# Performance work log

Measured on AMD Instinct MI355X. Metric: run time of the kernel, lower is better.

## Reference

```python
import jax, jax.numpy as jnp
import numpy as np

EMB = 1024
HEADS = 16
HEADSIZE = EMB // HEADS


def _layernorm(x, gamma, beta, eps=1e-5):
    # LayerNorm over the last dim (headsize), affine.
    mu = jnp.mean(x, axis=-1, keepdims=True)
    var = jnp.var(x, axis=-1, keepdims=True)
    return (x - mu) * jax.lax.rsqrt(var + eps) * gamma + beta


def setup_inputs() -> dict:
    key = jax.random.key(0)
    ks = jax.random.split(key, 12)
    B, TI, TC = 4, 1024, 1024
    s = 1.0 / np.sqrt(EMB)
    inp = {
        "x": jax.random.normal(ks[0], (B, TI, EMB), dtype=jnp.float32),
        "context": jax.random.normal(ks[1], (B, TC, EMB), dtype=jnp.float32),
        # torch nn.Linear weights are (out, in); y = x @ W.T
        "Wq": jax.random.uniform(ks[2], (EMB, EMB), jnp.float32, -s, s),
        "Wk": jax.random.uniform(ks[3], (EMB, EMB), jnp.float32, -s, s),
        "Wv": jax.random.uniform(ks[4], (EMB, EMB), jnp.float32, -s, s),
        "Wu": jax.random.uniform(ks[5], (EMB, EMB), jnp.float32, -s, s),
        "bu": jax.random.uniform(ks[6], (EMB,), jnp.float32, -s, s),
        "q_gamma": jnp.ones((HEADSIZE,), jnp.float32),
        "q_beta": jnp.zeros((HEADSIZE,), jnp.float32),
        "k_gamma": jnp.ones((HEADSIZE,), jnp.float32),
        "k_beta": jnp.zeros((HEADSIZE,), jnp.float32),
    }
    return inp


def reference(x, context, Wq, Wk, Wv, Wu, bu, q_gamma, q_beta, k_gamma, k_beta):
    B, TI, E = x.shape
    TC = context.shape[1]
    T = TI + TC
    xc = jnp.concatenate([x, context], axis=1)  # [B, T, E]

    q = (x @ Wq.T).reshape(B, TI, HEADS, HEADSIZE)
    k = (xc @ Wk.T).reshape(B, T, HEADS, HEADSIZE)
    v = (xc @ Wv.T).reshape(B, T, HEADS, HEADSIZE)

    # optional QK-LayerNorm over headsize
    q = _layernorm(q, q_gamma, q_beta)
    k = _layernorm(k, k_gamma, k_beta)

    scale = E ** 0.25
    q = q / scale
    k = k / scale

    # scores: [B, H, TI, T]
    dot = jnp.einsum("bihd,bjhd->bhij", q, k)
    attn = jax.nn.softmax(dot, axis=-1)
    out = jnp.einsum("bhij,bjhd->bihd", attn, v).reshape(B, TI, E)
    return out @ Wu.T + bu
```

## Files before the change

### kernel.cpp

```cpp
#include <hip/hip_runtime.h>
#include <cstdint>


typedef unsigned short u16;
typedef __attribute__((ext_vector_type(8))) short bf16x8;
typedef __attribute__((ext_vector_type(4))) float f32x4;
typedef __attribute__((ext_vector_type(16))) float f32x16;
typedef __attribute__((ext_vector_type(4))) unsigned short u16x4;
typedef __attribute__((ext_vector_type(2))) unsigned int u32x2;

#define GLDS(gsrc, ldst)                                                              \
  __builtin_amdgcn_global_load_lds(                                                   \
      (const __attribute__((address_space(1))) unsigned int*)(gsrc),                  \
      (__attribute__((address_space(3))) unsigned int*)(ldst), 16, 0, 0)

__device__ __forceinline__ u16 f2bf(float x) {
  unsigned int u = __float_as_uint(x);
  u += 0x7fffu + ((u >> 16) & 1u);
  return (u16)(u >> 16);
}

__device__ __forceinline__ unsigned cvt_pk_bf16(float lo, float hi) {
  unsigned r;
  asm("v_cvt_pk_bf16_f32 %0, %1, %2" : "=v"(r) : "v"(lo), "v"(hi));
  return r;
}

__device__ __forceinline__ f32x4 mfma16(bf16x8 a, bf16x8 b, f32x4 c) {
  return __builtin_amdgcn_mfma_f32_16x16x32_bf16(a, b, c, 0, 0, 0);
}
__device__ __forceinline__ f32x16 mfma32(bf16x8 a, bf16x8 b, f32x16 c) {
  return __builtin_amdgcn_mfma_f32_32x32x16_bf16(a, b, c, 0, 0, 0);
}


__global__ __launch_bounds__(256) void cast_concat(const float* __restrict__ x,
                                                   const float* __restrict__ c,
                                                   u16* __restrict__ o) {
  const int n4 = (8 << 20) / 4;
  for (int i = blockIdx.x * blockDim.x + threadIdx.x; i < n4; i += gridDim.x * blockDim.x) {
    int elem = i * 4;
    int b = elem >> 21;
    int rem = elem & ((1 << 21) - 1);
    int r = rem >> 10;
    int e = rem & 1023;
    const float* src = (r < 1024) ? (x + ((((size_t)(b << 10)) + r) << 10) + e)
                                  : (c + ((((size_t)(b << 10)) + (r - 1024)) << 10) + e);
    float4 v = *(const float4*)src;
    u16x4 ov;
    ov.x = f2bf(v.x); ov.y = f2bf(v.y); ov.z = f2bf(v.z); ov.w = f2bf(v.w);
    *(u16x4*)(o + elem) = ov;
  }
}

__global__ __launch_bounds__(256) void cast_w(const float* __restrict__ w0,
                                              const float* __restrict__ w1,
                                              const float* __restrict__ w2,
                                              const float* __restrict__ w3,
                                              u16* __restrict__ o) {
  const int n4 = (4 << 20) / 4;
  for (int i = blockIdx.x * blockDim.x + threadIdx.x; i < n4; i += gridDim.x * blockDim.x) {
    int elem = i * 4;
    int sel = elem >> 20;
    int loc = elem & ((1 << 20) - 1);
    const float* s = (sel == 0) ? w0 : (sel == 1) ? w1 : (sel == 2) ? w2 : w3;
    float4 v = *(const float4*)(s + loc);
    u16x4 ov;
    ov.x = f2bf(v.x); ov.y = f2bf(v.y); ov.z = f2bf(v.z); ov.w = f2bf(v.w);
    *(u16x4*)(o + elem) = ov;
  }
}


__global__ __launch_bounds__(256)
void gemm_qkv(const u16* __restrict__ XCB, const u16* __restrict__ Wall,
              u16* __restrict__ QBB, u16* __restrict__ KBB, u16* __restrict__ VT,
              const float* __restrict__ qg, const float* __restrict__ qb,
              const float* __restrict__ kg, const float* __restrict__ kb,
              float sQ, float sK) {
  const int ny = blockIdx.y;
  const int which = ny >> 3;
  const int m0 = blockIdx.x << 7;
  if (which == 0 && (m0 & 2047) >= 1024) return;
  const int n0 = (ny & 7) << 7;
  const u16* Bw = Wall + ((size_t)which << 20);
  const int K = 1024, N = 1024;

  __shared__ alignas(16) u16 lA[2][128 * 32];
  __shared__ alignas(16) u16 lB[2][128 * 32];
  const int tid = threadIdx.x;
  const int wv = tid >> 6, l = tid & 63, g = l >> 4, c16 = l & 15;
  const int wr = wv >> 1, wc = wv & 1;

  f32x4 acc[4][4];
  const f32x4 z4 = {0.f, 0.f, 0.f, 0.f};
#pragma unroll
  for (int i = 0; i < 4; ++i)
#pragma unroll
    for (int j = 0; j < 4; ++j) acc[i][j] = z4;

  const int srow = tid >> 2;
  const int scA = (tid & 3) ^ (srow & 3);
  const u16* aSrc = XCB + (size_t)(m0 + srow) * K + scA * 8;
  const u16* bSrc = Bw + (size_t)(n0 + srow) * K + scA * 8;
  char* ldA = (char*)lA;
  char* ldB = (char*)lB;
  const int lof = wv * 1024;

#define STAGE_G(bi, kof)                                   \
  {                                                        \
    char* dA = ldA + (bi)*8192 + lof;                      \
    char* dB = ldB + (bi)*8192 + lof;                      \
    GLDS(aSrc + (kof), dA);                                \
    GLDS(aSrc + (size_t)64 * K + (kof), dA + 4096);        \
    GLDS(bSrc + (kof), dB);                                \
    GLDS(bSrc + (size_t)64 * K + (kof), dB + 4096);        \
  }

  STAGE_G(0, 0);
  __syncthreads();
  int buf = 0;
  for (int kt = 0; kt < 32; ++kt) {
    if (kt + 1 < 32) STAGE_G(buf ^ 1, (kt + 1) << 5);
    const char* bA = ldA + buf * 8192;
    const char* bB = ldB + buf * 8192;
    bf16x8 af[4], bfr[4];
#pragma unroll
    for (int mi = 0; mi < 4; ++mi) {
      int row = wr * 64 + mi * 16 + c16;
      af[mi] = *(const bf16x8*)(bA + row * 64 + ((g * 16) ^ ((row & 3) << 4)));
    }
#pragma unroll
    for (int ni = 0; ni < 4; ++ni) {
      int row = wc * 64 + ni * 16 + c16;
      bfr[ni] = *(const bf16x8*)(bB + row * 64 + ((g * 16) ^ ((row & 3) << 4)));
    }
    __builtin_amdgcn_s_setprio(1);
#pragma unroll
    for (int mi = 0; mi < 4; ++mi)
#pragma unroll
      for (int ni = 0; ni < 4; ++ni)
        acc[mi][ni] = mfma16(af[mi], bfr[ni], acc[mi][ni]);
    __builtin_amdgcn_s_setprio(0);
    __syncthreads();
    buf ^= 1;
  }
#undef STAGE_G

  if (which == 2) {
#pragma unroll
    for (int ni = 0; ni < 4; ++ni) {
      int col = n0 + wc * 64 + ni * 16 + c16;
      int hh = col >> 6, dd = col & 63;
#pragma unroll
      for (int mi = 0; mi < 4; ++mi) {
        int m = m0 + wr * 64 + mi * 16 + g * 4;
        int bb = m >> 11, tt = m & 2047;
        u16x4 o;
#pragma unroll
        for (int r = 0; r < 4; ++r) o[r] = f2bf(acc[mi][ni][r]);
        *(u16x4*)(VT + ((size_t)((bb * 16 + hh) * 64 + dd)) * 2048 + tt) = o;
      }
    }
  } else {
    const float* G = which ? kg : qg;
    const float* Bt = which ? kb : qb;
    const float osc = which ? sK : sQ;
    u16* Ob = which ? KBB : QBB;
#pragma unroll
    for (int mi = 0; mi < 4; ++mi) {
      float sum[4], sq[4];
#pragma unroll
      for (int r = 0; r < 4; ++r) {
        float s = 0.f, q = 0.f;
#pragma unroll
        for (int ni = 0; ni < 4; ++ni) {
          float v = acc[mi][ni][r];
          s += v;
          q += v * v;
        }
#pragma unroll
        for (int msk = 1; msk < 16; msk <<= 1) {
          s += __shfl_xor(s, msk);
          q += __shfl_xor(q, msk);
        }
        sum[r] = s;
        sq[r] = q;
      }
#pragma unroll
      for (int ni = 0; ni < 4; ++ni) {
        int dloc = ni * 16 + c16;
        int colg = n0 + wc * 64 + ni * 16 + c16;
        float gv = G[dloc], bv = Bt[dloc];
#pragma unroll
        for (int r = 0; r < 4; ++r) {
          float mean = sum[r] * (1.f / 64.f);
          float var = sq[r] * (1.f / 64.f) - mean * mean;
          float y = (acc[mi][ni][r] - mean) * rsqrtf(var + 1e-5f) * gv + bv;
          int row = m0 + wr * 64 + mi * 16 + g * 4 + r;
          int orow = which ? row : (((row >> 11) << 10) | (row & 1023));
          Ob[(size_t)orow * N + colg] = f2bf(y * osc);
        }
      }
    }
  }
}


__global__ __launch_bounds__(256)
void gemm_u64(const u16* __restrict__ A, const u16* __restrict__ Bw,
              float* __restrict__ Of, const float* __restrict__ bias) {
  const int K = 1024, N = 1024;
  __shared__ alignas(16) u16 lA[2][64 * 32];
  __shared__ alignas(16) u16 lB[2][128 * 32];
  const int tid = threadIdx.x;
  const int wv = tid >> 6, l = tid & 63, g = l >> 4, c16 = l & 15;
  const int wr = wv >> 1, wc = wv & 1;
  const int m0 = blockIdx.x << 6, n0 = blockIdx.y << 7;

  f32x4 acc[2][4];
  const f32x4 z4 = {0.f, 0.f, 0.f, 0.f};
#pragma unroll
  for (int i = 0; i < 2; ++i)
#pragma unroll
    for (int j = 0; j < 4; ++j) acc[i][j] = z4;

  const int srow = tid >> 2;
  const int sc = (tid & 3) ^ (srow & 3);
  const u16* aSrc = A + (size_t)(m0 + srow) * K + sc * 8;
  const u16* bSrc = Bw + (size_t)(n0 + srow) * K + sc * 8;
  char* ldA = (char*)lA;
  char* ldB = (char*)lB;
  const int lof = wv * 1024;

#define STAGE_U(bi, kof)                                   \
  {                                                        \
    char* dA = ldA + (bi)*4096 + lof;                      \
    char* dB = ldB + (bi)*8192 + lof;                      \
    GLDS(aSrc + (kof), dA);                                \
    GLDS(bSrc + (kof), dB);                                \
    GLDS(bSrc + (size_t)64 * K + (kof), dB + 4096);        \
  }

  STAGE_U(0, 0);
  __syncthreads();
  int buf = 0;
  for (int kt = 0; kt < 32; ++kt) {
    if (kt + 1 < 32) STAGE_U(buf ^ 1, (kt + 1) << 5);
    const char* bA = ldA + buf * 4096;
    const char* bB = ldB + buf * 8192;
    bf16x8 af[2], bfr[4];
#pragma unroll
    for (int mi = 0; mi < 2; ++mi) {
      int row = wr * 32 + mi * 16 + c16;
      af[mi] = *(const bf16x8*)(bA + row * 64 + ((g * 16) ^ ((row & 3) << 4)));
    }
#pragma unroll
    for (int ni = 0; ni < 4; ++ni) {
      int row = wc * 64 + ni * 16 + c16;
      bfr[ni] = *(const bf16x8*)(bB + row * 64 + ((g * 16) ^ ((row & 3) << 4)));
    }
    __builtin_amdgcn_s_setprio(1);
#pragma unroll
    for (int mi = 0; mi < 2; ++mi)
#pragma unroll
      for (int ni = 0; ni < 4; ++ni)
        acc[mi][ni] = mfma16(af[mi], bfr[ni], acc[mi][ni]);
    __builtin_amdgcn_s_setprio(0);
    __syncthreads();
    buf ^= 1;
  }
#undef STAGE_U

#pragma unroll
  for (int ni = 0; ni < 4; ++ni) {
    int col = n0 + wc * 64 + ni * 16 + c16;
    float bv = bias[col];
#pragma unroll
    for (int mi = 0; mi < 2; ++mi) {
      int row = m0 + wr * 32 + mi * 16 + g * 4;
      float* dst = Of + (size_t)row * N + col;
#pragma unroll
      for (int r = 0; r < 4; ++r) dst[(size_t)r * N] = acc[mi][ni][r] + bv;
    }
  }
}


__global__ __launch_bounds__(512, 4)
void attn_kernel(const u16* __restrict__ Q, const u16* __restrict__ Kb,
                 const u16* __restrict__ Vt, u16* __restrict__ AO) {
  __shared__ union alignas(16) {
    struct { u16 K[2][2][4096]; u16 V[2][2][4096]; } kv;
    float cmb[4][64][34];
  } sm;
  const int tid = threadIdx.x;
  const int wv = tid >> 6, l = tid & 63;
  const int w4 = wv & 3, kvh2 = wv >> 2;
  const int lq = l & 31, hi = l >> 5;
  const int b = blockIdx.z, h = blockIdx.y, qt = blockIdx.x;
  const int qrow = (b << 10) + (qt << 7) + (w4 << 5) + lq;

  const u16* qp = Q + (size_t)qrow * 1024 + h * 64 + hi * 8;
  bf16x8 qf[4];
#pragma unroll
  for (int kk = 0; kk < 4; ++kk) qf[kk] = *(const bf16x8*)(qp + 16 * kk);

  f32x16 acc[2];
#pragma unroll
  for (int d0 = 0; d0 < 2; ++d0)
#pragma unroll
    for (int i = 0; i < 16; ++i) acc[d0][i] = 0.f;
  float m_run = -1e30f, l_run = 0.f;

  const u16* Ksrc = Kb + ((size_t)(b * 2048) + l) * 1024 + h * 64 + w4 * 8;
  const u16* Vsrc = Vt + ((size_t)((b * 16 + h) * 64) + l) * 2048 + w4 * 8;

#define STAGE_KV(bi, it)                                    \
  {                                                         \
    const int kv0 = ((it) << 7) + (kvh2 << 6);              \
    char* dK = (char*)sm.kv.K[kvh2][bi] + w4 * 1024;        \
    char* dV = (char*)sm.kv.V[kvh2][bi] + w4 * 1024;        \
    const u16* ks = Ksrc + (size_t)kv0 * 1024;              \
    const u16* vs = Vsrc + kv0;                             \
    GLDS(ks, dK);                                           \
    GLDS(ks + 32, dK + 4096);                               \
    GLDS(vs, dV);                                           \
    GLDS(vs + 32, dV + 4096);                               \
  }

  STAGE_KV(0, 0);
  __syncthreads();
  int buf = 0;

  for (int it = 0; it < 16; ++it) {
    if (it + 1 < 16) STAGE_KV(buf ^ 1, it + 1);
    const char* bK = (const char*)sm.kv.K[kvh2][buf];
    const char* bV = (const char*)sm.kv.V[kvh2][buf];

    f32x16 s[2];
#pragma unroll
    for (int kvh = 0; kvh < 2; ++kvh)
#pragma unroll
      for (int i = 0; i < 16; ++i) s[kvh][i] = 0.f;
    __builtin_amdgcn_s_setprio(1);
#pragma unroll
    for (int kk = 0; kk < 4; ++kk) {
      const char* kbase = bK + (2 * kk + hi) * 1024;
      bf16x8 kf0 = *(const bf16x8*)(kbase + lq * 16);
      bf16x8 kf1 = *(const bf16x8*)(kbase + (32 + lq) * 16);
      s[0] = mfma32(kf0, qf[kk], s[0]);
      s[1] = mfma32(kf1, qf[kk], s[1]);
    }
    __builtin_amdgcn_s_setprio(0);

    float tm0 = fmaxf(s[0][0], s[1][0]), tm1 = fmaxf(s[0][1], s[1][1]);
    float tm2 = fmaxf(s[0][2], s[1][2]), tm3 = fmaxf(s[0][3], s[1][3]);
#pragma unroll
    for (int i = 4; i < 16; i += 4) {
      tm0 = fmaxf(tm0, fmaxf(s[0][i], s[1][i]));
      tm1 = fmaxf(tm1, fmaxf(s[0][i + 1], s[1][i + 1]));
      tm2 = fmaxf(tm2, fmaxf(s[0][i + 2], s[1][i + 2]));
      tm3 = fmaxf(tm3, fmaxf(s[0][i + 3], s[1][i + 3]));
    }
    float tm = fmaxf(fmaxf(tm0, tm1), fmaxf(tm2, tm3));
    tm = fmaxf(tm, __shfl_xor(tm, 32));
    if (!__all(tm <= m_run + 8.f)) {
      float mnew = fmaxf(m_run, tm);
      float corr = __builtin_amdgcn_exp2f(m_run - mnew);
      l_run *= corr;
#pragma unroll
      for (int d0 = 0; d0 < 2; ++d0)
#pragma unroll
        for (int i = 0; i < 16; ++i) acc[d0][i] *= corr;
      m_run = mnew;
    }
    float ts0 = 0.f, ts1 = 0.f, ts2 = 0.f, ts3 = 0.f;
#pragma unroll
    for (int kvh = 0; kvh < 2; ++kvh)
#pragma unroll
      for (int i = 0; i < 16; i += 4) {
        float p0 = __builtin_amdgcn_exp2f(s[kvh][i] - m_run);
        float p1 = __builtin_amdgcn_exp2f(s[kvh][i + 1] - m_run);
        float p2 = __builtin_amdgcn_exp2f(s[kvh][i + 2] - m_run);
        float p3 = __builtin_amdgcn_exp2f(s[kvh][i + 3] - m_run);
        s[kvh][i] = p0; s[kvh][i + 1] = p1; s[kvh][i + 2] = p2; s[kvh][i + 3] = p3;
        ts0 += p0; ts1 += p1; ts2 += p2; ts3 += p3;
      }
    float ts = (ts0 + ts1) + (ts2 + ts3);
    ts += __shfl_xor(ts, 32);
    l_run += ts;

    unsigned int pk[2][4][2];
#pragma unroll
    for (int kvh = 0; kvh < 2; ++kvh)
#pragma unroll
      for (int kp = 0; kp < 4; ++kp)
#pragma unroll
        for (int tt = 0; tt < 2; ++tt)
          pk[kvh][kp][tt] = cvt_pk_bf16(s[kvh][4 * kp + 2 * tt], s[kvh][4 * kp + 2 * tt + 1]);

    __builtin_amdgcn_s_setprio(1);
#pragma unroll
    for (int kk = 0; kk < 4; ++kk) {
      const int kvh = kk >> 1, kb = kk & 1;
      union { unsigned w[4]; bf16x8 v; } bw;
#pragma unroll
      for (int tt = 0; tt < 2; ++tt) {
        unsigned A0 = pk[kvh][2 * kb][tt];
        unsigned A1 = pk[kvh][2 * kb + 1][tt];
        unsigned S = (unsigned)__shfl_xor((int)(hi ? A0 : A1), 32);
        bw.w[tt] = hi ? S : A0;
        bw.w[2 + tt] = hi ? A1 : S;
      }
      const char* vbase = bV + (2 * kk + hi) * 1024;
      bf16x8 vf0 = *(const bf16x8*)(vbase + lq * 16);
      bf16x8 vf1 = *(const bf16x8*)(vbase + (32 + lq) * 16);
      acc[0] = mfma32(vf0, bw.v, acc[0]);
      acc[1] = mfma32(vf1, bw.v, acc[1]);
    }
    __builtin_amdgcn_s_setprio(0);
    __syncthreads();
    buf ^= 1;
  }
#undef STAGE_KV

  if (wv >= 4) {
    float* cp = sm.cmb[w4][l];
#pragma unroll
    for (int d0 = 0; d0 < 2; ++d0)
#pragma unroll
      for (int i = 0; i < 16; ++i) cp[d0 * 16 + i] = acc[d0][i];
    cp[32] = m_run;
    cp[33] = l_run;
  }
  __syncthreads();
  if (wv < 4) {
    const float* cp = sm.cmb[w4][l];
    float m1 = cp[32], l1 = cp[33];
    float mm = fmaxf(m_run, m1);
    float c0 = __builtin_amdgcn_exp2f(m_run - mm);
    float c1 = __builtin_amdgcn_exp2f(m1 - mm);
    float invl = 1.f / (l_run * c0 + l1 * c1);
    float s0 = c0 * invl, s1 = c1 * invl;
#pragma unroll
    for (int d0 = 0; d0 < 2; ++d0)
#pragma unroll
      for (int rg = 0; rg < 4; ++rg) {
        float v0 = acc[d0][4 * rg + 0] * s0 + cp[d0 * 16 + 4 * rg + 0] * s1;
        float v1 = acc[d0][4 * rg + 1] * s0 + cp[d0 * 16 + 4 * rg + 1] * s1;
        float v2 = acc[d0][4 * rg + 2] * s0 + cp[d0 * 16 + 4 * rg + 2] * s1;
        float v3 = acc[d0][4 * rg + 3] * s0 + cp[d0 * 16 + 4 * rg + 3] * s1;
        u32x2 o;
        o.x = cvt_pk_bf16(v0, v1);
        o.y = cvt_pk_bf16(v2, v3);
        int d = 32 * d0 + 8 * rg + 4 * hi;
        *(u32x2*)(AO + (size_t)qrow * 1024 + h * 64 + d) = o;
      }
  }
}


extern "C" void kernel_launch(void* const* d_in, const int* in_sizes, int n_in,
                              void* d_out, int out_size, void* d_ws, size_t ws_size,
                              hipStream_t stream) {
  const float* x = (const float*)d_in[0];
  const float* ctx = (const float*)d_in[1];
  const float* Wq = (const float*)d_in[2];
  const float* Wk = (const float*)d_in[3];
  const float* Wv = (const float*)d_in[4];
  const float* Wu = (const float*)d_in[5];
  const float* bu = (const float*)d_in[6];
  const float* qg = (const float*)d_in[7];
  const float* qb = (const float*)d_in[8];
  const float* kg = (const float*)d_in[9];
  const float* kb = (const float*)d_in[10];
  float* out = (float*)d_out;

  char* w = (char*)d_ws;
  u16* XCB = (u16*)(w);
  u16* WQB = (u16*)(w + ((size_t)16 << 20));
  u16* QBB = (u16*)(w + ((size_t)24 << 20));
  u16* KBB = (u16*)(w + ((size_t)32 << 20));
  u16* VT = (u16*)(w + ((size_t)48 << 20));
  u16* AO = (u16*)(w + ((size_t)64 << 20));

  const float invs = 0.17677669529663687f;
  const float invs_l2e = invs * 1.44269504088896f;

  cast_concat<<<2048, 256, 0, stream>>>(x, ctx, XCB);
  cast_w<<<1024, 256, 0, stream>>>(Wq, Wk, Wv, Wu, WQB);

  gemm_qkv<<<dim3(64, 24), 256, 0, stream>>>(XCB, WQB, QBB, KBB, VT,
                                             qg, qb, kg, kb, invs_l2e, invs);

  attn_kernel<<<dim3(8, 16, 4), 512, 0, stream>>>(QBB, KBB, VT, AO);

  gemm_u64<<<dim3(64, 8), 256, 0, stream>>>(AO, WQB + ((size_t)3 << 20), out, bu);
}
```

Baseline: 276.5 us.

## Triple-buffer GEMM LDS staging with vmcnt waits and k-major LDS layout; reorder attention grid

Both projection GEMMs now stage three K-tiles in LDS instead of two. They issue loads two steps ahead and wait with explicit s_waitcnt vmcnt plus a single barrier per iteration, rather than two __syncthreads. The LDS layout moves from swizzled row-major to k-chunk-major, where each wave writes one 8-element k-slice for 64 rows, so fragment reads no longer need the XOR swizzle. The attention grid is reordered so heads vary fastest, with the aim of improving K/V cache reuse across neighbouring blocks. The extra buffer uses more LDS, which may limit occupancy, and the new layout may bring back bank conflicts.

```diff
diff --git a/kernel.cpp b/kernel.cpp
--- a/kernel.cpp
+++ b/kernel.cpp
@@ -86,8 +86,8 @@
   const u16* Bw = Wall + ((size_t)which << 20);
   const int K = 1024, N = 1024;
 
-  __shared__ alignas(16) u16 lA[2][128 * 32];
-  __shared__ alignas(16) u16 lB[2][128 * 32];
+  __shared__ alignas(16) u16 lAm[3][128 * 32];
+  __shared__ alignas(16) u16 lBm[3][128 * 32];
   const int tid = threadIdx.x;
   const int wv = tid >> 6, l = tid & 63, g = l >> 4, c16 = l & 15;
   const int wr = wv >> 1, wc = wv & 1;
@@ -99,42 +99,41 @@
 #pragma unroll
     for (int j = 0; j < 4; ++j) acc[i][j] = z4;
 
-  const int srow = tid >> 2;
-  const int scA = (tid & 3) ^ (srow & 3);
-  const u16* aSrc = XCB + (size_t)(m0 + srow) * K + scA * 8;
-  const u16* bSrc = Bw + (size_t)(n0 + srow) * K + scA * 8;
-  char* ldA = (char*)lA;
-  char* ldB = (char*)lB;
-  const int lof = wv * 1024;
+  const u16* aSrc = XCB + (size_t)(m0 + l) * K + wv * 8;
+  const u16* bSrc = Bw + (size_t)(n0 + l) * K + wv * 8;
+  char* ldA = (char*)lAm;
+  char* ldB = (char*)lBm;
 
 #define STAGE_G(bi, kof)                                   \
   {                                                        \
-    char* dA = ldA + (bi)*8192 + lof;                      \
-    char* dB = ldB + (bi)*8192 + lof;                      \
+    char* dA = ldA + (bi)*8192 + wv * 2048;                \
+    char* dB = ldB + (bi)*8192 + wv * 2048;                \
     GLDS(aSrc + (kof), dA);                                \
-    GLDS(aSrc + (size_t)64 * K + (kof), dA + 4096);        \
+    GLDS(aSrc + (size_t)64 * K + (kof), dA + 1024);        \
     GLDS(bSrc + (kof), dB);                                \
-    GLDS(bSrc + (size_t)64 * K + (kof), dB + 4096);        \
+    GLDS(bSrc + (size_t)64 * K + (kof), dB + 1024);        \
   }
 
   STAGE_G(0, 0);
-  __syncthreads();
-  int buf = 0;
+  STAGE_G(1, 32);
+  int cb = 0, sb = 2;
   for (int kt = 0; kt < 32; ++kt) {
-    if (kt + 1 < 32) STAGE_G(buf ^ 1, (kt + 1) << 5);
-    const char* bA = ldA + buf * 8192;
-    const char* bB = ldB + buf * 8192;
+    if (kt < 31) {
+      asm volatile("s_waitcnt vmcnt(4)" ::: "memory");
+    } else {
+      asm volatile("s_waitcnt vmcnt(0)" ::: "memory");
+    }
+    __builtin_amdgcn_s_barrier();
+    if (kt + 2 < 32) STAGE_G(sb, (kt + 2) << 5);
+    const char* bA = ldA + cb * 8192;
+    const char* bB = ldB + cb * 8192;
     bf16x8 af[4], bfr[4];
 #pragma unroll
-    for (int mi = 0; mi < 4; ++mi) {
-      int row = wr * 64 + mi * 16 + c16;
-      af[mi] = *(const bf16x8*)(bA + row * 64 + ((g * 16) ^ ((row & 3) << 4)));
-    }
-#pragma unroll
-    for (int ni = 0; ni < 4; ++ni) {
-      int row = wc * 64 + ni * 16 + c16;
-      bfr[ni] = *(const bf16x8*)(bB + row * 64 + ((g * 16) ^ ((row & 3) << 4)));
-    }
+    for (int mi = 0; mi < 4; ++mi)
+      af[mi] = *(const bf16x8*)(bA + g * 2048 + (wr * 64 + mi * 16 + c16) * 16);
+#pragma unroll
+    for (int ni = 0; ni < 4; ++ni)
+      bfr[ni] = *(const bf16x8*)(bB + g * 2048 + (wc * 64 + ni * 16 + c16) * 16);
     __builtin_amdgcn_s_setprio(1);
 #pragma unroll
     for (int mi = 0; mi < 4; ++mi)
@@ -142,8 +141,8 @@
       for (int ni = 0; ni < 4; ++ni)
         acc[mi][ni] = mfma16(af[mi], bfr[ni], acc[mi][ni]);
     __builtin_amdgcn_s_setprio(0);
-    __syncthreads();
-    buf ^= 1;
+    cb = cb == 2 ? 0 : cb + 1;
+    sb = sb == 2 ? 0 : sb + 1;
   }
 #undef STAGE_G
 
@@ -211,8 +210,8 @@
 void gemm_u64(const u16* __restrict__ A, const u16* __restrict__ Bw,
               float* __restrict__ Of, const float* __restrict__ bias) {
   const int K = 1024, N = 1024;
-  __shared__ alignas(16) u16 lA[2][64 * 32];
-  __shared__ alignas(16) u16 lB[2][128 * 32];
+  __shared__ alignas(16) u16 lAm[3][64 * 32];
+  __shared__ alignas(16) u16 lBm[3][128 * 32];
   const int tid = threadIdx.x;
   const int wv = tid >> 6, l = tid & 63, g = l >> 4, c16 = l & 15;
   const int wr = wv >> 1, wc = wv & 1;
@@ -225,41 +224,40 @@
 #pragma unroll
     for (int j = 0; j < 4; ++j) acc[i][j] = z4;
 
-  const int srow = tid >> 2;
-  const int sc = (tid & 3) ^ (srow & 3);
-  const u16* aSrc = A + (size_t)(m0 + srow) * K + sc * 8;
-  const u16* bSrc = Bw + (size_t)(n0 + srow) * K + sc * 8;
-  char* ldA = (char*)lA;
-  char* ldB = (char*)lB;
-  const int lof = wv * 1024;
+  const u16* aSrc = A + (size_t)(m0 + l) * K + wv * 8;
+  const u16* bSrc = Bw + (size_t)(n0 + l) * K + wv * 8;
+  char* ldA = (char*)lAm;
+  char* ldB = (char*)lBm;
 
 #define STAGE_U(bi, kof)                                   \
   {                                                        \
-    char* dA = ldA + (bi)*4096 + lof;                      \
-    char* dB = ldB + (bi)*8192 + lof;                      \
+    char* dA = ldA + (bi)*4096 + wv * 1024;                \
+    char* dB = ldB + (bi)*8192 + wv * 2048;                \
     GLDS(aSrc + (kof), dA);                                \
     GLDS(bSrc + (kof), dB);                                \
-    GLDS(bSrc + (size_t)64 * K + (kof), dB + 4096);        \
+    GLDS(bSrc + (size_t)64 * K + (kof), dB + 1024);        \
   }
 
   STAGE_U(0, 0);
-  __syncthreads();
-  int buf = 0;
+  STAGE_U(1, 32);
+  int cb = 0, sb = 2;
   for (int kt = 0; kt < 32; ++kt) {
-    if (kt + 1 < 32) STAGE_U(buf ^ 1, (kt + 1) << 5);
-    const char* bA = ldA + buf * 4096;
-    const char* bB = ldB + buf * 8192;
+    if (kt < 31) {
+      asm volatile("s_waitcnt vmcnt(3)" ::: "memory");
+    } else {
+      asm volatile("s_waitcnt vmcnt(0)" ::: "memory");
+    }
+    __builtin_amdgcn_s_barrier();
+    if (kt + 2 < 32) STAGE_U(sb, (kt + 2) << 5);
+    const char* bA = ldA + cb * 4096;
+    const char* bB = ldB + cb * 8192;
     bf16x8 af[2], bfr[4];
 #pragma unroll
-    for (int mi = 0; mi < 2; ++mi) {
-      int row = wr * 32 + mi * 16 + c16;
-      af[mi] = *(const bf16x8*)(bA + row * 64 + ((g * 16) ^ ((row & 3) << 4)));
-    }
-#pragma unroll
-    for (int ni = 0; ni < 4; ++ni) {
-      int row = wc * 64 + ni * 16 + c16;
-      bfr[ni] = *(const bf16x8*)(bB + row * 64 + ((g * 16) ^ ((row & 3) << 4)));
-    }
+    for (int mi = 0; mi < 2; ++mi)
+      af[mi] = *(const bf16x8*)(bA + g * 1024 + (wr * 32 + mi * 16 + c16) * 16);
+#pragma unroll
+    for (int ni = 0; ni < 4; ++ni)
+      bfr[ni] = *(const bf16x8*)(bB + g * 2048 + (wc * 64 + ni * 16 + c16) * 16);
     __builtin_amdgcn_s_setprio(1);
 #pragma unroll
     for (int mi = 0; mi < 2; ++mi)
@@ -267,8 +265,8 @@
       for (int ni = 0; ni < 4; ++ni)
         acc[mi][ni] = mfma16(af[mi], bfr[ni], acc[mi][ni]);
     __builtin_amdgcn_s_setprio(0);
-    __syncthreads();
-    buf ^= 1;
+    cb = cb == 2 ? 0 : cb + 1;
+    sb = sb == 2 ? 0 : sb + 1;
   }
 #undef STAGE_U
 
@@ -298,7 +296,7 @@
   const int wv = tid >> 6, l = tid & 63;
   const int w4 = wv & 3, kvh2 = wv >> 2;
   const int lq = l & 31, hi = l >> 5;
-  const int b = blockIdx.z, h = blockIdx.y, qt = blockIdx.x;
+  const int h = blockIdx.x, b = blockIdx.y, qt = blockIdx.z;
   const int qrow = (b << 10) + (qt << 7) + (w4 << 5) + lq;
 
   const u16* qp = Q + (size_t)qrow * 1024 + h * 64 + hi * 8;
@@ -494,7 +492,7 @@
   gemm_qkv<<<dim3(64, 24), 256, 0, stream>>>(XCB, WQB, QBB, KBB, VT,
                                              qg, qb, kg, kb, invs_l2e, invs);
 
-  attn_kernel<<<dim3(8, 16, 4), 512, 0, stream>>>(QBB, KBB, VT, AO);
+  attn_kernel<<<dim3(16, 4, 8), 512, 0, stream>>>(QBB, KBB, VT, AO);
 
   gemm_u64<<<dim3(64, 8), 256, 0, stream>>>(AO, WQB + ((size_t)3 << 20), out, bu);
 }
```

Result: slower. 295.1 us (+6.7%).
